# Kernel optimization log

Measured on AMD Instinct MI355X. Metric: run time of the kernel, lower is better.

## Reference

```python
import jax, jax.numpy as jnp
import numpy as np

N = 100000   # nodes
E = 1600000  # edges
D = 64       # feature dim (input = hidden = output)
G = 256      # graphs in batch
EPS = 1e-5   # BatchNorm eps


def setup_inputs() -> dict:
    key = jax.random.key(0)
    ks = jax.random.split(key, 16)
    inp = {
        "x": jax.random.normal(ks[0], (N, D), dtype=jnp.float32),
        "edge_index": jax.random.randint(ks[1], (2, E), 0, N, dtype=jnp.int64),
        "batch": jnp.sort(jax.random.randint(ks[2], (N,), 0, G, dtype=jnp.int64)),
    }
    # GCNConv weights (glorot-ish) + biases, and BatchNorm affine params, 3 layers
    for i in range(3):
        inp[f"W{i+1}"] = jax.random.normal(ks[3 + i], (D, D), dtype=jnp.float32) / np.sqrt(D)
        inp[f"b{i+1}"] = jnp.zeros((D,), dtype=jnp.float32)
        inp[f"g{i+1}"] = jnp.ones((D,), dtype=jnp.float32)   # BN gamma
        inp[f"be{i+1}"] = jnp.zeros((D,), dtype=jnp.float32)  # BN beta
    return inp


def _batchnorm(x, gamma, beta):
    # BatchNorm1d in training mode: batch stats over the node dim (biased var)
    mean = jnp.mean(x, axis=0)
    var = jnp.mean(jnp.square(x - mean), axis=0)
    return (x - mean) * jax.lax.rsqrt(var + EPS) * gamma + beta


def reference(x, edge_index, batch, W1, b1, g1, be1, W2, b2, g2, be2, W3, b3, g3, be3):
    src, dst = edge_index[0], edge_index[1]
    # GCN normalization with self-loops: norm_ij = deg_i^-1/2 * deg_j^-1/2 over A + I
    loop = jnp.arange(N, dtype=src.dtype)
    src2 = jnp.concatenate([src, loop])
    dst2 = jnp.concatenate([dst, loop])
    deg = jax.ops.segment_sum(jnp.ones_like(src2, dtype=x.dtype), dst2, num_segments=N)
    dinv = jax.lax.rsqrt(deg)  # deg >= 1 thanks to self loops
    norm = (dinv[src2] * dinv[dst2])[:, None]  # [E+N, 1]

    def gcn_conv(h, W, b):
        h = h @ W                                   # [N, D] small GEMM
        msg = h[src2] * norm                        # per-edge gather (memory bound)
        return jax.ops.segment_sum(msg, dst2, num_segments=N) + b

    params = [(W1, b1, g1, be1), (W2, b2, g2, be2), (W3, b3, g3, be3)]
    h = x
    for i, (W, b, g, be) in enumerate(params):
        h = gcn_conv(h, W, b)
        h = _batchnorm(h, g, be)
        if i < 2:
            h = jax.nn.relu(h)
            # dropout(p=0.2) is identity in deterministic/eval reference

    # global mean + max pool per graph
    ones = jnp.ones((N,), dtype=h.dtype)
    cnt = jax.ops.segment_sum(ones, batch, num_segments=G)            # [G]
    s = jax.ops.segment_sum(h, batch, num_segments=G)                 # [G, D]
    mean = s / jnp.maximum(cnt, 1.0)[:, None]
    mx = jax.ops.segment_max(h, batch, num_segments=G)
    mx = jnp.where(cnt[:, None] > 0, mx, 0.0)
    return mean + mx
```

## Files before the change

### kernel.cpp

```cpp
#include <hip/hip_runtime.h>
#include <hip/hip_bf16.h>
#include <math.h>

#define N_NODES 100000
#define N_EDGES 1600000
#define DIM 64
#define N_GRAPHS 256
#define BN_EPS 1e-5f
#define N_XCD 8
#define BUCKET ((N_NODES + N_XCD - 1) / N_XCD)
#define FILL_CHUNKS 128
#define FILL_ESIZE ((N_EDGES + FILL_CHUNKS - 1) / FILL_CHUNKS)
#define CSR_STRIDE 48
#define HIST_BLOCKS (FILL_CHUNKS * N_XCD)
#define GEMM0_BLOCKS 1024

__device__ inline unsigned short f2bf(float f) {
    __hip_bfloat16 h = __float2bfloat16(f);
    return *reinterpret_cast<unsigned short*>(&h);
}
__device__ inline unsigned int pack2bf(float a, float b) {
    return (unsigned int)f2bf(a) | ((unsigned int)f2bf(b) << 16);
}
__device__ inline float bf_lo(unsigned int u) { return __uint_as_float(u << 16); }
__device__ inline float bf_hi(unsigned int u) { return __uint_as_float(u & 0xffff0000u); }

__global__ __launch_bounds__(256) void hist_gemm0(const int* __restrict__ src,
                                                  const int* __restrict__ dst,
                                                  int* __restrict__ cnt,
                                                  int* __restrict__ csr_pad,
                                                  const float* __restrict__ x,
                                                  const float* __restrict__ W,
                                                  unsigned short* __restrict__ tb) {
    if (blockIdx.x < HIST_BLOCKS) {
        int chunk = blockIdx.x >> 3;
        int lo = (blockIdx.x & (N_XCD - 1)) * BUCKET;
        int e0 = chunk * FILL_ESIZE;
        int e1 = min(e0 + FILL_ESIZE, N_EDGES);
        for (int e = e0 + threadIdx.x; e < e1; e += 256) {
            int d = __builtin_nontemporal_load(&dst[e]);
            if ((unsigned)(d - lo) < (unsigned)BUCKET) {
                int r = atomicAdd(&cnt[d], 1);
                csr_pad[d * CSR_STRIDE + r] = __builtin_nontemporal_load(&src[e]);
            }
        }
    } else {
        int tid = threadIdx.x;
        int d = tid & 63;
        int wv = tid >> 6;
        float wcol[64];
        #pragma unroll
        for (int k = 0; k < 64; ++k) wcol[k] = W[k * 64 + d];
        int gb = blockIdx.x - HIST_BLOCKS;
        int nwaves = GEMM0_BLOCKS * 4;
        for (int row = gb * 4 + wv; row < N_NODES; row += nwaves) {
            int urow = __builtin_amdgcn_readfirstlane(row);
            const float* hr = x + (size_t)urow * 64;
            float a0 = 0.f, a1 = 0.f, a2 = 0.f, a3 = 0.f;
            #pragma unroll
            for (int k = 0; k < 64; k += 4) {
                a0 = fmaf(hr[k + 0], wcol[k + 0], a0);
                a1 = fmaf(hr[k + 1], wcol[k + 1], a1);
                a2 = fmaf(hr[k + 2], wcol[k + 2], a2);
                a3 = fmaf(hr[k + 3], wcol[k + 3], a3);
            }
            float acc = (a0 + a1) + (a2 + a3);
            tb[(size_t)urow * 64 + d] = f2bf(acc);
        }
    }
}

__global__ __launch_bounds__(256) void finish_scale(const int* __restrict__ cnt,
                                                    unsigned short* __restrict__ tb,
                                                    float* __restrict__ dinv) {
    const int total = N_NODES * 8;
    for (int i = blockIdx.x * 256 + threadIdx.x; i < total; i += gridDim.x * 256) {
        int row = i >> 3;
        float di = rsqrtf((float)(cnt[row] + 1));
        uint4 u = *reinterpret_cast<const uint4*>(tb + (size_t)i * 8);
        uint4 o;
        o.x = pack2bf(bf_lo(u.x) * di, bf_hi(u.x) * di);
        o.y = pack2bf(bf_lo(u.y) * di, bf_hi(u.y) * di);
        o.z = pack2bf(bf_lo(u.z) * di, bf_hi(u.z) * di);
        o.w = pack2bf(bf_lo(u.w) * di, bf_hi(u.w) * di);
        *reinterpret_cast<uint4*>(tb + (size_t)i * 8) = o;
        if ((i & 7) == 0) dinv[row] = di;
    }
}

__global__ __launch_bounds__(256) void gemm_f32(const float* __restrict__ h,
                                                const float* __restrict__ W,
                                                const float* __restrict__ dinv,
                                                unsigned short* __restrict__ tb) {
    int tid = threadIdx.x;
    int d = tid & 63;
    int wv = tid >> 6;
    float wcol[64];
    #pragma unroll
    for (int k = 0; k < 64; ++k) wcol[k] = W[k * 64 + d];
    int nwaves = gridDim.x * 4;
    for (int row = blockIdx.x * 4 + wv; row < N_NODES; row += nwaves) {
        int urow = __builtin_amdgcn_readfirstlane(row);
        const float* hr = h + (size_t)urow * 64;
        float a0 = 0.f, a1 = 0.f, a2 = 0.f, a3 = 0.f;
        #pragma unroll
        for (int k = 0; k < 64; k += 4) {
            a0 = fmaf(hr[k + 0], wcol[k + 0], a0);
            a1 = fmaf(hr[k + 1], wcol[k + 1], a1);
            a2 = fmaf(hr[k + 2], wcol[k + 2], a2);
            a3 = fmaf(hr[k + 3], wcol[k + 3], a3);
        }
        float acc = (a0 + a1) + (a2 + a3);
        tb[(size_t)urow * 64 + d] = f2bf(acc * dinv[urow]);
    }
}

__global__ __launch_bounds__(256) void bnrelu(const unsigned short* __restrict__ agg,
                                              const float* __restrict__ stats,
                                              const float* __restrict__ gamma,
                                              const float* __restrict__ beta,
                                              float* __restrict__ hp) {
    __shared__ float scale[64], shift[64];
    int tid = threadIdx.x;
    if (tid < 64) {
        const float inv_n = 1.0f / (float)N_NODES;
        float mean = stats[tid] * inv_n;
        float var = fmaxf(stats[64 + tid] * inv_n - mean * mean, 0.f);
        float rs = rsqrtf(var + BN_EPS) * gamma[tid];
        scale[tid] = rs;
        shift[tid] = beta[tid] - mean * rs;
    }
    __syncthreads();
    const size_t total = (size_t)N_NODES * 8;
    for (size_t i = (size_t)blockIdx.x * 256 + tid; i < total; i += (size_t)gridDim.x * 256) {
        uint4 u = *reinterpret_cast<const uint4*>(agg + i * 8);
        int dd = (int)((i * 8) & 63);
        float4 o0, o1;
        o0.x = fmaxf(fmaf(bf_lo(u.x), scale[dd + 0], shift[dd + 0]), 0.f);
        o0.y = fmaxf(fmaf(bf_hi(u.x), scale[dd + 1], shift[dd + 1]), 0.f);
        o0.z = fmaxf(fmaf(bf_lo(u.y), scale[dd + 2], shift[dd + 2]), 0.f);
        o0.w = fmaxf(fmaf(bf_hi(u.y), scale[dd + 3], shift[dd + 3]), 0.f);
        o1.x = fmaxf(fmaf(bf_lo(u.z), scale[dd + 4], shift[dd + 4]), 0.f);
        o1.y = fmaxf(fmaf(bf_hi(u.z), scale[dd + 5], shift[dd + 5]), 0.f);
        o1.z = fmaxf(fmaf(bf_lo(u.w), scale[dd + 6], shift[dd + 6]), 0.f);
        o1.w = fmaxf(fmaf(bf_hi(u.w), scale[dd + 7], shift[dd + 7]), 0.f);
        *reinterpret_cast<float4*>(hp + i * 8) = o0;
        *reinterpret_cast<float4*>(hp + i * 8 + 4) = o1;
    }
}

__global__ __launch_bounds__(256) void gather_agg(const int* __restrict__ csr_pad,
                                                  const int* __restrict__ cnt,
                                                  const float* __restrict__ dinv,
                                                  const unsigned short* __restrict__ tb,
                                                  const float* __restrict__ bias,
                                                  unsigned short* __restrict__ out,
                                                  float* __restrict__ stats) {
    int tid = threadIdx.x;
    int wave = tid >> 6;
    int lane = tid & 63;
    int q    = lane >> 4;
    int ql   = lane & 15;

    float4 s4  = {0.f, 0.f, 0.f, 0.f};
    float4 sq4 = {0.f, 0.f, 0.f, 0.f};

    for (int v = blockIdx.x * 4 + wave; v < N_NODES; v += gridDim.x * 4) {
        int beg = v * CSR_STRIDE;
        int end = beg + cnt[v];
        float4 acc  = {0.f, 0.f, 0.f, 0.f};
        float4 acc2 = {0.f, 0.f, 0.f, 0.f};
        int e = beg + q;
        for (; e + 4 < end; e += 8) {
            int s0 = csr_pad[e];
            int s1 = csr_pad[e + 4];
            uint2 u0 = *reinterpret_cast<const uint2*>(tb + (size_t)s0 * 64 + ql * 4);
            uint2 u1 = *reinterpret_cast<const uint2*>(tb + (size_t)s1 * 64 + ql * 4);
            acc.x  += bf_lo(u0.x); acc.y  += bf_hi(u0.x);
            acc.z  += bf_lo(u0.y); acc.w  += bf_hi(u0.y);
            acc2.x += bf_lo(u1.x); acc2.y += bf_hi(u1.x);
            acc2.z += bf_lo(u1.y); acc2.w += bf_hi(u1.y);
        }
        if (e < end) {
            int s0 = csr_pad[e];
            uint2 u0 = *reinterpret_cast<const uint2*>(tb + (size_t)s0 * 64 + ql * 4);
            acc.x += bf_lo(u0.x); acc.y += bf_hi(u0.x);
            acc.z += bf_lo(u0.y); acc.w += bf_hi(u0.y);
        }
        acc.x += acc2.x; acc.y += acc2.y; acc.z += acc2.z; acc.w += acc2.w;

        acc.x += __shfl_xor(acc.x, 16, 64); acc.x += __shfl_xor(acc.x, 32, 64);
        acc.y += __shfl_xor(acc.y, 16, 64); acc.y += __shfl_xor(acc.y, 32, 64);
        acc.z += __shfl_xor(acc.z, 16, 64); acc.z += __shfl_xor(acc.z, 32, 64);
        acc.w += __shfl_xor(acc.w, 16, 64); acc.w += __shfl_xor(acc.w, 32, 64);

        if (q == 0) {
            float di = dinv[v];
            uint2 uv = *reinterpret_cast<const uint2*>(tb + (size_t)v * 64 + ql * 4);
            float4 bi = *reinterpret_cast<const float4*>(bias + ql * 4);
            float4 val;
            val.x = fmaf(di, acc.x + bf_lo(uv.x), bi.x);
            val.y = fmaf(di, acc.y + bf_hi(uv.x), bi.y);
            val.z = fmaf(di, acc.z + bf_lo(uv.y), bi.z);
            val.w = fmaf(di, acc.w + bf_hi(uv.y), bi.w);
            uint2 o;
            o.x = pack2bf(val.x, val.y);
            o.y = pack2bf(val.z, val.w);
            *reinterpret_cast<uint2*>(out + (size_t)v * 64 + ql * 4) = o;
            s4.x += val.x; s4.y += val.y; s4.z += val.z; s4.w += val.w;
            sq4.x += val.x * val.x; sq4.y += val.y * val.y;
            sq4.z += val.z * val.z; sq4.w += val.w * val.w;
        }
    }

    __shared__ float shs[4][64];
    __shared__ float shq[4][64];
    if (q == 0) {
        *reinterpret_cast<float4*>(&shs[wave][ql * 4]) = s4;
        *reinterpret_cast<float4*>(&shq[wave][ql * 4]) = sq4;
    }
    __syncthreads();
    if (tid < 64) {
        float S = shs[0][tid] + shs[1][tid] + shs[2][tid] + shs[3][tid];
        float Q = shq[0][tid] + shq[1][tid] + shq[2][tid] + shq[3][tid];
        unsafeAtomicAdd(&stats[tid], S);
        unsafeAtomicAdd(&stats[64 + tid], Q);
    }
}

__global__ __launch_bounds__(256) void pool_partial(const unsigned short* __restrict__ hb,
                                                    const int* __restrict__ batch,
                                                    const float* __restrict__ stats,
                                                    const float* __restrict__ gamma,
                                                    const float* __restrict__ beta,
                                                    float* __restrict__ pS,
                                                    float* __restrict__ pM) {
    int bid = blockIdx.x;
    int g = bid >> 2, p = bid & 3;
    __shared__ float scale[64], shift[64];
    __shared__ int bounds[2];
    int tid = threadIdx.x;
    if (tid < 64) {
        const float inv_n = 1.0f / (float)N_NODES;
        float mean = stats[tid] * inv_n;
        float var = fmaxf(stats[64 + tid] * inv_n - mean * mean, 0.f);
        float rs = rsqrtf(var + BN_EPS) * gamma[tid];
        scale[tid] = rs;
        shift[tid] = beta[tid] - mean * rs;
    }
    if (tid < 2) {
        int target = g + tid;
        int lo = 0, hi = N_NODES;
        while (lo < hi) {
            int mid = (lo + hi) >> 1;
            if (batch[mid] < target) lo = mid + 1; else hi = mid;
        }
        bounds[tid] = lo;
    }
    __syncthreads();
    int lo = bounds[0], hi = bounds[1];
    int d = tid & 63, g4 = tid >> 6;
    float sc = scale[d], sh = shift[d];
    float s = 0.f, m = -3.402823466e38f;
    for (int row = lo + p * 4 + g4; row < hi; row += 16) {
        float v = __uint_as_float(((unsigned int)hb[(size_t)row * 64 + d]) << 16);
        v = fmaf(v, sc, sh);
        s += v;
        m = fmaxf(m, v);
    }
    __shared__ float shs[8][64];
    shs[g4][d] = s;
    shs[4 + g4][d] = m;
    __syncthreads();
    if (tid < 64) {
        float S = shs[0][tid] + shs[1][tid] + shs[2][tid] + shs[3][tid];
        float M = fmaxf(fmaxf(shs[4][tid], shs[5][tid]), fmaxf(shs[6][tid], shs[7][tid]));
        pS[bid * 64 + tid] = S;
        pM[bid * 64 + tid] = M;
    }
}

__global__ __launch_bounds__(64) void pool_final(const int* __restrict__ batch,
                                                 const float* __restrict__ pS,
                                                 const float* __restrict__ pM,
                                                 float* __restrict__ out) {
    int g = blockIdx.x, d = threadIdx.x;
    __shared__ int bounds[2];
    if (d < 2) {
        int target = g + d;
        int lo = 0, hi = N_NODES;
        while (lo < hi) {
            int mid = (lo + hi) >> 1;
            if (batch[mid] < target) lo = mid + 1; else hi = mid;
        }
        bounds[d] = lo;
    }
    __syncthreads();
    int cnt = bounds[1] - bounds[0];
    int base = g * 4 * 64 + d;
    float S = (pS[base] + pS[base + 64]) + (pS[base + 128] + pS[base + 192]);
    float M = fmaxf(fmaxf(pM[base], pM[base + 64]), fmaxf(pM[base + 128], pM[base + 192]));
    float mean = S / fmaxf((float)cnt, 1.0f);
    out[g * 64 + d] = (cnt > 0) ? (mean + M) : 0.0f;
}

extern "C" void kernel_launch(void* const* d_in, const int* in_sizes, int n_in,
                              void* d_out, int out_size, void* d_ws, size_t ws_size,
                              hipStream_t stream) {
    const float* x     = (const float*)d_in[0];
    const int*   eidx  = (const int*)d_in[1];
    const int*   batch = (const int*)d_in[2];
    const float* W[3]  = {(const float*)d_in[3], (const float*)d_in[7],  (const float*)d_in[11]};
    const float* b[3]  = {(const float*)d_in[4], (const float*)d_in[8],  (const float*)d_in[12]};
    const float* gm[3] = {(const float*)d_in[5], (const float*)d_in[9],  (const float*)d_in[13]};
    const float* be[3] = {(const float*)d_in[6], (const float*)d_in[10], (const float*)d_in[14]};

    float*          hp    = (float*)d_ws;
    unsigned short* tb    = (unsigned short*)(hp + (size_t)N_NODES * 64);
    unsigned short* agg   = tb + (size_t)N_NODES * 64;
    float* dinv     = (float*)(agg + (size_t)N_NODES * 64);
    float* stats    = dinv + N_NODES;
    float* poolS    = stats + 384;
    float* poolM    = poolS + 1024 * 64;
    int*   cnt      = (int*)(poolM + 1024 * 64);
    int*   csr_pad  = cnt + N_NODES;

    const int* srcp = eidx;
    const int* dstp = eidx + N_EDGES;

    hipMemsetAsync(stats, 0, 384 * sizeof(float), stream);
    hipMemsetAsync(cnt, 0, N_NODES * sizeof(int), stream);

    hist_gemm0<<<HIST_BLOCKS + GEMM0_BLOCKS, 256, 0, stream>>>(srcp, dstp, cnt, csr_pad,
                                                               x, W[0], tb);
    finish_scale<<<1024, 256, 0, stream>>>(cnt, tb, dinv);

    gather_agg<<<2048, 256, 0, stream>>>(csr_pad, cnt, dinv, tb, b[0], agg, stats);

    bnrelu<<<1024, 256, 0, stream>>>(agg, stats, gm[0], be[0], hp);
    gemm_f32<<<1024, 256, 0, stream>>>(hp, W[1], dinv, tb);
    gather_agg<<<2048, 256, 0, stream>>>(csr_pad, cnt, dinv, tb, b[1], agg, stats + 128);

    bnrelu<<<1024, 256, 0, stream>>>(agg, stats + 128, gm[1], be[1], hp);
    gemm_f32<<<1024, 256, 0, stream>>>(hp, W[2], dinv, tb);
    gather_agg<<<2048, 256, 0, stream>>>(csr_pad, cnt, dinv, tb, b[2], agg, stats + 256);

    pool_partial<<<N_GRAPHS * 4, 256, 0, stream>>>(agg, batch, stats + 256, gm[2], be[2], poolS, poolM);
    pool_final<<<N_GRAPHS, 64, 0, stream>>>(batch, poolS, poolM, (float*)d_out);
}
```

Baseline: 455.4 us.

## Fuse BatchNorm+ReLU into the following GEMM and merge workspace memsets

Replaces the separate bnrelu and gemm_f32 kernels with one kernel. It reads the bf16 aggregation, applies the BN scale/shift and ReLU per element, stages the activated row in per-wave LDS, then runs the 64x64 matvec against register-held W columns. This removes the fp32 hp intermediate write and read and one launch per layer. The workspace is reordered so stats and cnt sit next to each other and can be cleared with a single memset. The per-wave LDS staging relies on lockstep wave execution without a barrier.

```diff
diff --git a/kernel.cpp b/kernel.cpp
--- a/kernel.cpp
+++ b/kernel.cpp
@@ -88,64 +88,49 @@
     }
 }
 
-__global__ __launch_bounds__(256) void gemm_f32(const float* __restrict__ h,
-                                                const float* __restrict__ W,
-                                                const float* __restrict__ dinv,
-                                                unsigned short* __restrict__ tb) {
+__global__ __launch_bounds__(256) void bn_gemm_v(const unsigned short* __restrict__ hb,
+                                                 const float* __restrict__ stats,
+                                                 const float* __restrict__ gamma,
+                                                 const float* __restrict__ beta,
+                                                 const float* __restrict__ W,
+                                                 const float* __restrict__ dinv,
+                                                 unsigned short* __restrict__ tb) {
+    __shared__ float abuf[4][64];
+    __shared__ float scale_s[64], shift_s[64];
     int tid = threadIdx.x;
     int d = tid & 63;
     int wv = tid >> 6;
-    float wcol[64];
-    #pragma unroll
-    for (int k = 0; k < 64; ++k) wcol[k] = W[k * 64 + d];
-    int nwaves = gridDim.x * 4;
-    for (int row = blockIdx.x * 4 + wv; row < N_NODES; row += nwaves) {
-        int urow = __builtin_amdgcn_readfirstlane(row);
-        const float* hr = h + (size_t)urow * 64;
-        float a0 = 0.f, a1 = 0.f, a2 = 0.f, a3 = 0.f;
-        #pragma unroll
-        for (int k = 0; k < 64; k += 4) {
-            a0 = fmaf(hr[k + 0], wcol[k + 0], a0);
-            a1 = fmaf(hr[k + 1], wcol[k + 1], a1);
-            a2 = fmaf(hr[k + 2], wcol[k + 2], a2);
-            a3 = fmaf(hr[k + 3], wcol[k + 3], a3);
-        }
-        float acc = (a0 + a1) + (a2 + a3);
-        tb[(size_t)urow * 64 + d] = f2bf(acc * dinv[urow]);
-    }
-}
-
-__global__ __launch_bounds__(256) void bnrelu(const unsigned short* __restrict__ agg,
-                                              const float* __restrict__ stats,
-                                              const float* __restrict__ gamma,
-                                              const float* __restrict__ beta,
-                                              float* __restrict__ hp) {
-    __shared__ float scale[64], shift[64];
-    int tid = threadIdx.x;
     if (tid < 64) {
         const float inv_n = 1.0f / (float)N_NODES;
         float mean = stats[tid] * inv_n;
         float var = fmaxf(stats[64 + tid] * inv_n - mean * mean, 0.f);
         float rs = rsqrtf(var + BN_EPS) * gamma[tid];
-        scale[tid] = rs;
-        shift[tid] = beta[tid] - mean * rs;
-    }
-    __syncthreads();
-    const size_t total = (size_t)N_NODES * 8;
-    for (size_t i = (size_t)blockIdx.x * 256 + tid; i < total; i += (size_t)gridDim.x * 256) {
-        uint4 u = *reinterpret_cast<const uint4*>(agg + i * 8);
-        int dd = (int)((i * 8) & 63);
-        float4 o0, o1;
-        o0.x = fmaxf(fmaf(bf_lo(u.x), scale[dd + 0], shift[dd + 0]), 0.f);
-        o0.y = fmaxf(fmaf(bf_hi(u.x), scale[dd + 1], shift[dd + 1]), 0.f);
-        o0.z = fmaxf(fmaf(bf_lo(u.y), scale[dd + 2], shift[dd + 2]), 0.f);
-        o0.w = fmaxf(fmaf(bf_hi(u.y), scale[dd + 3], shift[dd + 3]), 0.f);
-        o1.x = fmaxf(fmaf(bf_lo(u.z), scale[dd + 4], shift[dd + 4]), 0.f);
-        o1.y = fmaxf(fmaf(bf_hi(u.z), scale[dd + 5], shift[dd + 5]), 0.f);
-        o1.z = fmaxf(fmaf(bf_lo(u.w), scale[dd + 6], shift[dd + 6]), 0.f);
-        o1.w = fmaxf(fmaf(bf_hi(u.w), scale[dd + 7], shift[dd + 7]), 0.f);
-        *reinterpret_cast<float4*>(hp + i * 8) = o0;
-        *reinterpret_cast<float4*>(hp + i * 8 + 4) = o1;
+        scale_s[tid] = rs;
+        shift_s[tid] = beta[tid] - mean * rs;
+    }
+    float wcol[64];
+    #pragma unroll
+    for (int k = 0; k < 64; ++k) wcol[k] = W[k * 64 + d];
+    __syncthreads();
+    float sc = scale_s[d], sh = shift_s[d];
+    const float4* av = reinterpret_cast<const float4*>(abuf[wv]);
+    int nwaves = gridDim.x * 4;
+    for (int row = blockIdx.x * 4 + wv; row < N_NODES; row += nwaves) {
+        float h = __uint_as_float(((unsigned int)hb[(size_t)row * 64 + d]) << 16);
+        float a = fmaxf(fmaf(h, sc, sh), 0.f);
+        abuf[wv][d] = a;
+        float a0 = 0.f, a1 = 0.f, a2 = 0.f, a3 = 0.f;
+        #pragma unroll
+        for (int k4 = 0; k4 < 16; ++k4) {
+            float4 v = av[k4];
+            int k = k4 * 4;
+            a0 = fmaf(v.x, wcol[k + 0], a0);
+            a1 = fmaf(v.y, wcol[k + 1], a1);
+            a2 = fmaf(v.z, wcol[k + 2], a2);
+            a3 = fmaf(v.w, wcol[k + 3], a3);
+        }
+        float acc = (a0 + a1) + (a2 + a3);
+        tb[(size_t)row * 64 + d] = f2bf(acc * dinv[row]);
     }
 }
 
@@ -315,21 +300,19 @@
     const float* gm[3] = {(const float*)d_in[5], (const float*)d_in[9],  (const float*)d_in[13]};
     const float* be[3] = {(const float*)d_in[6], (const float*)d_in[10], (const float*)d_in[14]};
 
-    float*          hp    = (float*)d_ws;
-    unsigned short* tb    = (unsigned short*)(hp + (size_t)N_NODES * 64);
+    unsigned short* tb    = (unsigned short*)d_ws;
     unsigned short* agg   = tb + (size_t)N_NODES * 64;
     float* dinv     = (float*)(agg + (size_t)N_NODES * 64);
     float* stats    = dinv + N_NODES;
-    float* poolS    = stats + 384;
+    int*   cnt      = (int*)(stats + 384);
+    float* poolS    = (float*)(cnt + N_NODES);
     float* poolM    = poolS + 1024 * 64;
-    int*   cnt      = (int*)(poolM + 1024 * 64);
-    int*   csr_pad  = cnt + N_NODES;
+    int*   csr_pad  = (int*)(poolM + 1024 * 64);
 
     const int* srcp = eidx;
     const int* dstp = eidx + N_EDGES;
 
-    hipMemsetAsync(stats, 0, 384 * sizeof(float), stream);
-    hipMemsetAsync(cnt, 0, N_NODES * sizeof(int), stream);
+    hipMemsetAsync(stats, 0, (384 + N_NODES) * sizeof(float), stream);
 
     hist_gemm0<<<HIST_BLOCKS + GEMM0_BLOCKS, 256, 0, stream>>>(srcp, dstp, cnt, csr_pad,
                                                                x, W[0], tb);
@@ -337,12 +320,10 @@
 
     gather_agg<<<2048, 256, 0, stream>>>(csr_pad, cnt, dinv, tb, b[0], agg, stats);
 
-    bnrelu<<<1024, 256, 0, stream>>>(agg, stats, gm[0], be[0], hp);
-    gemm_f32<<<1024, 256, 0, stream>>>(hp, W[1], dinv, tb);
+    bn_gemm_v<<<1024, 256, 0, stream>>>(agg, stats, gm[0], be[0], W[1], dinv, tb);
     gather_agg<<<2048, 256, 0, stream>>>(csr_pad, cnt, dinv, tb, b[1], agg, stats + 128);
 
-    bnrelu<<<1024, 256, 0, stream>>>(agg, stats + 128, gm[1], be[1], hp);
-    gemm_f32<<<1024, 256, 0, stream>>>(hp, W[2], dinv, tb);
+    bn_gemm_v<<<1024, 256, 0, stream>>>(agg, stats + 128, gm[1], be[1], W[2], dinv, tb);
     gather_agg<<<2048, 256, 0, stream>>>(csr_pad, cnt, dinv, tb, b[2], agg, stats + 256);
 
     pool_partial<<<N_GRAPHS * 4, 256, 0, stream>>>(agg, batch, stats + 256, gm[2], be[2], poolS, poolM);
```

Result: faster. 445.5 us (-2.2%).
